# Performance work log

Measured on AMD Instinct MI355X. Metric: run time of the kernel, lower is better.

## Reference

```python
import jax, jax.numpy as jnp
import numpy as np

KH = KW = 3
STRIDE = 1
ITERATIONS = 2
EPS = 1e-7


def _squash(s):
    # squash along last axis (capsule dim)
    sn = jnp.sum(s * s, axis=-1, keepdims=True)
    return (sn / (1.0 + sn)) * s / jnp.sqrt(sn + EPS)


def setup_inputs() -> dict:
    key = jax.random.key(0)
    k1, k2 = jax.random.split(key)
    x = jax.random.normal(k1, (4, 14, 14, 32, 8), dtype=jnp.float32)
    # W: [1,1,1,filters_out, caps_per_patch=3*3*32, dims_out=16, dims_in=8], stddev=0.1 init
    W = 0.1 * jax.random.normal(k2, (1, 1, 1, 32, 288, 16, 8), dtype=jnp.float32)
    return {"x": x, "W": W}


def reference(x, W):
    B, H, Wd, Fin, Din = x.shape
    Ho = (H - KH) // STRIDE + 1
    Wo = (Wd - KW) // STRIDE + 1
    # Patch extraction, channel order (kh, kw, Fin) to match tf.image.extract_patches
    patches = jnp.stack(
        [x[:, i:i + Ho * STRIDE:STRIDE, j:j + Wo * STRIDE:STRIDE]
         for i in range(KH) for j in range(KW)],
        axis=3,
    )  # [B,Ho,Wo,KH*KW,Fin,Din]
    patches = patches.reshape(B, Ho, Wo, KH * KW * Fin, Din)  # [B,Ho,Wo,C,Di]

    Wm = W[0, 0, 0]  # [F, C, Do, Di]
    F, C, Do, _ = Wm.shape
    # predictions[b,h,w,f,c,o] = sum_i W[f,c,o,i] * patches[b,h,w,c,i]
    preds = jnp.einsum('fcoi,bhwci->bhwfco', Wm, patches)

    logits = jnp.zeros((B, Ho, Wo, F, C), dtype=preds.dtype)
    outputs = jnp.zeros((B, Ho, Wo, F, Do), dtype=preds.dtype)
    for _ in range(ITERATIONS):
        # agreement = predictions^T @ outputs over the dims_out axis
        agreement = jnp.einsum('bhwfco,bhwfo->bhwfc', preds, outputs)
        logits = logits + agreement
        # NOTE: original code softmaxes over axis=3 (the filters_out axis)
        cc = jax.nn.softmax(logits, axis=3)  # [B,Ho,Wo,F,C]
        centroids = jnp.sum(cc[..., None] * preds, axis=4)  # [B,Ho,Wo,F,Do]
        outputs = _squash(centroids)
    return outputs
```

## Files before the change

### kernel.cpp

```cpp
#include <hip/hip_runtime.h>

#define NB   4
#define H_IN 14
#define W_IN 14
#define FIN  32
#define DI   8
#define F    32
#define C    288
#define DO   16
#define HO   12
#define WO   12
#define NPOS (NB*HO*WO)
#define EPS  1e-7f

#define CH   16
#define CC   (C/CH)
#define GP   4
#define GRID (CH*(NPOS/GP))

#define XELE  (NB*H_IN*W_IN*FIN*DI)
#define W2H_BYTES  ((size_t)F*C*DO*DI*2)
#define XH_BYTES   ((size_t)XELE*2)
#define CENT_BYTES ((size_t)NPOS*F*DO*4)
#define PART_BYTES ((size_t)CH*CENT_BYTES)
#define OUT1_BYTES CENT_BYTES

#define WBLK ((F*C*DO)/256)
#define XBLK ((XELE/4 + 255)/256)

typedef _Float16 h2 __attribute__((ext_vector_type(2)));

__device__ __forceinline__ unsigned int pack2(float a, float b) {
    h2 v; v.x = (_Float16)a; v.y = (_Float16)b;
    return __builtin_bit_cast(unsigned int, v);
}

__device__ __forceinline__ float dot8h(const uint4 w, const uint4 v, float acc) {
#if __has_builtin(__builtin_amdgcn_fdot2)
    acc = __builtin_amdgcn_fdot2(__builtin_bit_cast(h2, w.x), __builtin_bit_cast(h2, v.x), acc, false);
    acc = __builtin_amdgcn_fdot2(__builtin_bit_cast(h2, w.y), __builtin_bit_cast(h2, v.y), acc, false);
    acc = __builtin_amdgcn_fdot2(__builtin_bit_cast(h2, w.z), __builtin_bit_cast(h2, v.z), acc, false);
    acc = __builtin_amdgcn_fdot2(__builtin_bit_cast(h2, w.w), __builtin_bit_cast(h2, v.w), acc, false);
#else
    const h2 w0 = __builtin_bit_cast(h2, w.x), v0 = __builtin_bit_cast(h2, v.x);
    const h2 w1 = __builtin_bit_cast(h2, w.y), v1 = __builtin_bit_cast(h2, v.y);
    const h2 w2 = __builtin_bit_cast(h2, w.z), v2 = __builtin_bit_cast(h2, v.z);
    const h2 w3 = __builtin_bit_cast(h2, w.w), v3 = __builtin_bit_cast(h2, v.w);
    acc += (float)w0.x*(float)v0.x + (float)w0.y*(float)v0.y
         + (float)w1.x*(float)v1.x + (float)w1.y*(float)v1.y
         + (float)w2.x*(float)v2.x + (float)w2.y*(float)v2.y
         + (float)w3.x*(float)v3.x + (float)w3.y*(float)v3.y;
#endif
    return acc;
}

__device__ __forceinline__ int xbase_of(int pos) {
    const int b = pos/(HO*WO), rem = pos%(HO*WO), ho = rem/WO, wo = rem%WO;
    return ((b*H_IN + ho)*W_IN + wo)*FIN*DI;
}

__device__ __forceinline__ int coff_of(int c) {
    const int slab = c >> 5, fin = c & 31;
    const int kh = slab/3, kw = slab%3;
    return (kh*W_IN + kw)*FIN*DI + fin*DI;
}

__global__ __launch_bounds__(256) void kernConv(const float* __restrict__ Wt,
                                                unsigned short* __restrict__ W2h,
                                                const float* __restrict__ x,
                                                unsigned short* __restrict__ xh) {
    const int b = blockIdx.x;
    if (b < WBLK) {
        const int idx = b*256 + threadIdx.x;
        const int f = idx & 31, o = (idx >> 5) & 15, c = idx >> 9;
        const float* src = Wt + ((size_t)(f*C + c)*DO + o)*DI;
        const float4 a = *(const float4*)src;
        const float4 bb = *(const float4*)(src + 4);
        uint4 r;
        r.x = pack2(a.x, a.y);  r.y = pack2(a.z, a.w);
        r.z = pack2(bb.x, bb.y); r.w = pack2(bb.z, bb.w);
        ((uint4*)W2h)[idx] = r;
    } else {
        const int i = (b - WBLK)*256 + threadIdx.x;
        if (i < XELE/4) {
            const float4 v = ((const float4*)x)[i];
            uint2 o;
            o.x = pack2(v.x, v.y); o.y = pack2(v.z, v.w);
            ((uint2*)xh)[i] = o;
        }
    }
}

__global__ __launch_bounds__(256, 8) void kern1n(const unsigned short* __restrict__ xh,
                                                 const unsigned short* __restrict__ W2h,
                                                 float* __restrict__ part1)
{
    const int tid = threadIdx.x;
    const int f  = tid & 31;
    const int og = tid >> 5;
    const int o0 = 2*og, o1 = o0 + 1;
    const int ch = blockIdx.x & (CH-1);
    const int pg = blockIdx.x >> 4;

    int xoff[GP];
    #pragma unroll
    for (int p = 0; p < GP; ++p) xoff[p] = xbase_of(pg*GP + p);

    const uint4* W2h4 = (const uint4*)W2h;
    const int c0 = ch*CC;

    float acc0[GP], acc1[GP];
    #pragma unroll
    for (int p = 0; p < GP; ++p) { acc0[p] = 0.f; acc1[p] = 0.f; }

    #pragma unroll 1
    for (int cl = 0; cl < CC; ++cl) {
        const int c = c0 + cl;
        const int coff = coff_of(c);
        const uint4 w0 = W2h4[(size_t)(c*DO + o0)*F + f];
        const uint4 w1 = W2h4[(size_t)(c*DO + o1)*F + f];
        #pragma unroll
        for (int p = 0; p < GP; ++p) {
            const uint4 xv = *(const uint4*)(xh + xoff[p] + coff);
            acc0[p] = dot8h(w0, xv, acc0[p]);
            acc1[p] = dot8h(w1, xv, acc1[p]);
        }
    }
    #pragma unroll
    for (int p = 0; p < GP; ++p) {
        const size_t base = ((size_t)(ch*NPOS + pg*GP + p))*DO;
        part1[(base + o0)*F + f] = acc0[p];
        part1[(base + o1)*F + f] = acc1[p];
    }
}

__global__ __launch_bounds__(512) void kernO(const float* __restrict__ part1,
                                             float* __restrict__ out1)
{
    __shared__ float red[512];
    const int pos = blockIdx.x, tid = threadIdx.x;
    const int f = tid & 31, o = tid >> 5;

    float s = 0.f;
    #pragma unroll
    for (int k = 0; k < CH; ++k)
        s += part1[(size_t)(k*NPOS + pos)*512 + tid];
    s *= (1.f/32.f);

    red[tid] = s*s;
    __syncthreads();
    if (tid < 256) red[tid] += red[tid + 256];
    __syncthreads();
    if (tid < 128) red[tid] += red[tid + 128];
    __syncthreads();
    if (tid < 64)  red[tid] += red[tid + 64];
    __syncthreads();
    if (tid < 32) {
        const float sn = red[tid] + red[tid + 32];
        red[tid] = (sn/(1.f + sn)) * rsqrtf(sn + EPS);
    }
    __syncthreads();
    out1[(size_t)pos*512 + f*DO + o] = s * red[f];
}

__global__ __launch_bounds__(256, 8) void kern2n(const unsigned short* __restrict__ xh,
                                                 const unsigned short* __restrict__ W2h,
                                                 const float* __restrict__ out1,
                                                 float* __restrict__ part2)
{
    __shared__ float red[2][4][GP][32];
    __shared__ float ccs[2][GP][32];

    const int tid = threadIdx.x;
    const int f  = tid & 31;
    const int og = tid >> 5;
    const int o0 = 2*og, o1 = o0 + 1;
    const int wv = tid >> 6;
    const int half = (tid >> 5) & 1;
    const int ch = blockIdx.x & (CH-1);
    const int pg = blockIdx.x >> 4;

    int xoff[GP];
    #pragma unroll
    for (int p = 0; p < GP; ++p) xoff[p] = xbase_of(pg*GP + p);

    float u0[GP], u1[GP];
    #pragma unroll
    for (int p = 0; p < GP; ++p) {
        const float* up = out1 + (size_t)(pg*GP + p)*512 + f*DO;
        u0[p] = up[o0];
        u1[p] = up[o1];
    }

    const uint4* W2h4 = (const uint4*)W2h;
    const int c0 = ch*CC;

    float acc0[GP], acc1[GP];
    #pragma unroll
    for (int p = 0; p < GP; ++p) { acc0[p] = 0.f; acc1[p] = 0.f; }

    #pragma unroll 1
    for (int cl = 0; cl < CC; ++cl) {
        const int c = c0 + cl;
        const int buf = cl & 1;
        const int coff = coff_of(c);
        const uint4 w0 = W2h4[(size_t)(c*DO + o0)*F + f];
        const uint4 w1 = W2h4[(size_t)(c*DO + o1)*F + f];

        float pred0[GP], pred1[GP];
        #pragma unroll
        for (int p = 0; p < GP; ++p) {
            const uint4 xv = *(const uint4*)(xh + xoff[p] + coff);
            pred0[p] = dot8h(w0, xv, 0.f);
            pred1[p] = dot8h(w1, xv, 0.f);
        }

        #pragma unroll
        for (int p = 0; p < GP; ++p) {
            float ap = pred0[p]*u0[p] + pred1[p]*u1[p];
            ap += __shfl_xor(ap, 32);
            if (half == 0) red[buf][wv][p][f] = ap;
        }
        __syncthreads();

        {
            const int p2 = tid >> 5, f2 = tid & 31;
            if (p2 < GP) {
                const float agr = red[buf][0][p2][f2] + red[buf][1][p2][f2]
                                + red[buf][2][p2][f2] + red[buf][3][p2][f2];
                float m = agr;
                m = fmaxf(m, __shfl_xor(m, 1));
                m = fmaxf(m, __shfl_xor(m, 2));
                m = fmaxf(m, __shfl_xor(m, 4));
                m = fmaxf(m, __shfl_xor(m, 8));
                m = fmaxf(m, __shfl_xor(m, 16));
                const float e = __expf(agr - m);
                float s = e;
                s += __shfl_xor(s, 1);
                s += __shfl_xor(s, 2);
                s += __shfl_xor(s, 4);
                s += __shfl_xor(s, 8);
                s += __shfl_xor(s, 16);
                ccs[buf][p2][f2] = e / s;
            }
        }
        __syncthreads();

        #pragma unroll
        for (int p = 0; p < GP; ++p) {
            const float cv = ccs[buf][p][f];
            acc0[p] += cv*pred0[p];
            acc1[p] += cv*pred1[p];
        }
    }

    #pragma unroll
    for (int p = 0; p < GP; ++p) {
        const size_t base = ((size_t)(ch*NPOS + pg*GP + p))*DO;
        part2[(base + o0)*F + f] = acc0[p];
        part2[(base + o1)*F + f] = acc1[p];
    }
}

__global__ __launch_bounds__(256) void kern3(const float* __restrict__ part2,
                                             float* __restrict__ out)
{
    const int tid = threadIdx.x;
    const int f = tid & 31, p = tid >> 5;
    const int pos = blockIdx.x*8 + p;

    float cent[DO];
    #pragma unroll
    for (int o = 0; o < DO; ++o) cent[o] = 0.f;
    #pragma unroll 1
    for (int k = 0; k < CH; ++k) {
        const float* s = part2 + (size_t)(k*NPOS + pos)*512 + f;
        #pragma unroll
        for (int o = 0; o < DO; ++o) cent[o] += s[o*F];
    }
    float sn = 0.f;
    #pragma unroll
    for (int o = 0; o < DO; ++o) sn += cent[o]*cent[o];
    const float sc = (sn/(1.f + sn)) * rsqrtf(sn + EPS);
    float* dst = out + ((size_t)pos*F + f)*DO;
    #pragma unroll
    for (int o = 0; o < DO; ++o) dst[o] = cent[o]*sc;
}

__device__ __forceinline__ float dot8(const float4* __restrict__ w,
                                      const float4 p0, const float4 p1) {
    float4 a = w[0], b = w[1];
    return a.x*p0.x + a.y*p0.y + a.z*p0.z + a.w*p0.w
         + b.x*p1.x + b.y*p1.y + b.z*p1.z + b.w*p1.w;
}

__global__ __launch_bounds__(256) void capsule_kernel_f32(
    const float* __restrict__ x, const float* __restrict__ Wt,
    float* __restrict__ out)
{
    __shared__ float patch[C*DI];
    __shared__ float cent[F*DO];
    __shared__ float out1[F*DO];
    __shared__ float agr[F*C];
    __shared__ float scale_s[F];

    const int tid = threadIdx.x;
    const int pos = blockIdx.x;
    const int b   = pos / (HO*WO);
    const int rem = pos % (HO*WO);
    const int ho  = rem / WO;
    const int wo  = rem % WO;

    #pragma unroll
    for (int slab = 0; slab < 9; ++slab) {
        const int kh = slab / 3, kw = slab % 3;
        const float* src = x + (((b*H_IN + ho + kh)*W_IN + (wo + kw))*FIN)*DI;
        patch[slab*256 + tid] = src[tid];
    }
    __syncthreads();

    const float4* pv = (const float4*)patch;

    {
        const int fo0 = tid, fo1 = tid + 256;
        const int f0 = fo0 >> 4, o0 = fo0 & 15;
        const int f1 = fo1 >> 4, o1 = fo1 & 15;
        float acc0 = 0.f, acc1 = 0.f;
        for (int c = 0; c < C; ++c) {
            const float4 p0 = pv[c*2], p1 = pv[c*2+1];
            acc0 += dot8((const float4*)(Wt + ((f0*C + c)*DO + o0)*DI), p0, p1);
            acc1 += dot8((const float4*)(Wt + ((f1*C + c)*DO + o1)*DI), p0, p1);
        }
        cent[fo0] = acc0 * (1.f/32.f);
        cent[fo1] = acc1 * (1.f/32.f);
    }
    __syncthreads();

    if (tid < F) {
        float sn = 0.f;
        #pragma unroll
        for (int o = 0; o < DO; ++o) { float v = cent[tid*DO + o]; sn += v*v; }
        const float sc = (sn/(1.f + sn)) * rsqrtf(sn + EPS);
        #pragma unroll
        for (int o = 0; o < DO; ++o) out1[tid*DO + o] = cent[tid*DO + o] * sc;
    }
    __syncthreads();

    #pragma unroll 1
    for (int r = 0; r < (F*C)/256; ++r) {
        const int pp = tid + 256*r;
        const int f = pp / C, c = pp % C;
        const float4* wrow = (const float4*)(Wt + (f*C + c)*DO*DI);
        const float4 p0 = pv[c*2], p1 = pv[c*2+1];
        float a = 0.f;
        #pragma unroll
        for (int o = 0; o < DO; ++o) a += dot8(wrow + o*2, p0, p1) * out1[f*DO + o];
        agr[pp] = a;
    }
    __syncthreads();

    for (int c = tid; c < C; c += 256) {
        float m = -1e30f;
        #pragma unroll
        for (int f = 0; f < F; ++f) m = fmaxf(m, agr[f*C + c]);
        float s = 0.f;
        #pragma unroll
        for (int f = 0; f < F; ++f) {
            const float e = __expf(agr[f*C + c] - m);
            agr[f*C + c] = e; s += e;
        }
        const float inv = 1.f / s;
        #pragma unroll
        for (int f = 0; f < F; ++f) agr[f*C + c] *= inv;
    }
    __syncthreads();

    {
        const int fo0 = tid, fo1 = tid + 256;
        const int f0 = fo0 >> 4, o0 = fo0 & 15;
        const int f1 = fo1 >> 4, o1 = fo1 & 15;
        float acc0 = 0.f, acc1 = 0.f;
        for (int c = 0; c < C; ++c) {
            const float4 p0 = pv[c*2], p1 = pv[c*2+1];
            acc0 += agr[f0*C + c] * dot8((const float4*)(Wt + ((f0*C + c)*DO + o0)*DI), p0, p1);
            acc1 += agr[f1*C + c] * dot8((const float4*)(Wt + ((f1*C + c)*DO + o1)*DI), p0, p1);
        }
        cent[fo0] = acc0;
        cent[fo1] = acc1;
    }
    __syncthreads();

    if (tid < F) {
        float sn = 0.f;
        #pragma unroll
        for (int o = 0; o < DO; ++o) { float v = cent[tid*DO + o]; sn += v*v; }
        scale_s[tid] = (sn/(1.f + sn)) * rsqrtf(sn + EPS);
    }
    __syncthreads();

    out[pos*(F*DO) + tid]       = cent[tid]       * scale_s[tid >> 4];
    out[pos*(F*DO) + tid + 256] = cent[tid + 256] * scale_s[(tid >> 4) + 16];
}

extern "C" void kernel_launch(void* const* d_in, const int* in_sizes, int n_in,
                              void* d_out, int out_size, void* d_ws, size_t ws_size,
                              hipStream_t stream) {
    const float* x  = (const float*)d_in[0];
    const float* Wt = (const float*)d_in[1];
    float* out = (float*)d_out;

    if (ws_size >= W2H_BYTES + XH_BYTES + PART_BYTES + OUT1_BYTES) {
        unsigned short* W2h = (unsigned short*)d_ws;
        unsigned short* xh  = (unsigned short*)((char*)d_ws + W2H_BYTES);
        float* part = (float*)((char*)d_ws + W2H_BYTES + XH_BYTES);
        float* out1 = (float*)((char*)d_ws + W2H_BYTES + XH_BYTES + PART_BYTES);
        kernConv<<<WBLK + XBLK, 256, 0, stream>>>(Wt, W2h, x, xh);
        kern1n<<<GRID, 256, 0, stream>>>(xh, W2h, part);
        kernO<<<NPOS, 512, 0, stream>>>(part, out1);
        kern2n<<<GRID, 256, 0, stream>>>(xh, W2h, out1, part);
        kern3<<<NPOS/8, 256, 0, stream>>>(part, out);
    } else {
        capsule_kernel_f32<<<NPOS, 256, 0, stream>>>(x, Wt, out);
    }
}
```

Baseline: 144.9 us.

## Compute first routing iteration with MFMA over pre-extracted fp16 patches

Replaces the first-iteration dot-product kernel and its separate reduce/squash kernel with one MFMA-based kernel. It computes the uniform-weight centroid as a GEMM over all 288×8 inputs per filter and fuses the squash in-register. The conversion kernel now also writes a plain fp16 copy of W and a materialized fp16 patch matrix, and kern2n reads the patch matrix with linear offsets. GP doubles to 8, so the softmax stage uses all threads. The cost is a larger workspace and extra conversion traffic, and kern2n now carries more per-thread state.

```diff
diff --git a/kernel.cpp b/kernel.cpp
--- a/kernel.cpp
+++ b/kernel.cpp
@@ -15,20 +15,25 @@
 
 #define CH   16
 #define CC   (C/CH)
-#define GP   4
+#define GP   8
 #define GRID (CH*(NPOS/GP))
 
-#define XELE  (NB*H_IN*W_IN*FIN*DI)
+#define KTOT (C*DI)
+
 #define W2H_BYTES  ((size_t)F*C*DO*DI*2)
-#define XH_BYTES   ((size_t)XELE*2)
-#define CENT_BYTES ((size_t)NPOS*F*DO*4)
-#define PART_BYTES ((size_t)CH*CENT_BYTES)
-#define OUT1_BYTES CENT_BYTES
-
-#define WBLK ((F*C*DO)/256)
-#define XBLK ((XELE/4 + 255)/256)
+#define WH_BYTES   ((size_t)F*C*DO*DI*2)
+#define PH_BYTES   ((size_t)NPOS*KTOT*2)
+#define PART_BYTES ((size_t)CH*NPOS*F*DO*4)
+#define OUT1_BYTES ((size_t)NPOS*F*DO*4)
+
+#define CVT_W2H 576
+#define CVT_WH  576
+#define CVT_PH  648
+#define CVT_GRID (CVT_W2H + CVT_WH + CVT_PH)
 
 typedef _Float16 h2 __attribute__((ext_vector_type(2)));
+typedef _Float16 h8v __attribute__((ext_vector_type(8)));
+typedef float    f4v __attribute__((ext_vector_type(4)));
 
 __device__ __forceinline__ unsigned int pack2(float a, float b) {
     h2 v; v.x = (_Float16)a; v.y = (_Float16)b;
@@ -66,107 +71,85 @@
 }
 
 __global__ __launch_bounds__(256) void kernConv(const float* __restrict__ Wt,
+                                                const float* __restrict__ x,
                                                 unsigned short* __restrict__ W2h,
-                                                const float* __restrict__ x,
-                                                unsigned short* __restrict__ xh) {
+                                                unsigned short* __restrict__ Wh,
+                                                unsigned short* __restrict__ Ph) {
     const int b = blockIdx.x;
-    if (b < WBLK) {
+    if (b < CVT_W2H) {
         const int idx = b*256 + threadIdx.x;
         const int f = idx & 31, o = (idx >> 5) & 15, c = idx >> 9;
         const float* src = Wt + ((size_t)(f*C + c)*DO + o)*DI;
         const float4 a = *(const float4*)src;
         const float4 bb = *(const float4*)(src + 4);
         uint4 r;
-        r.x = pack2(a.x, a.y);  r.y = pack2(a.z, a.w);
+        r.x = pack2(a.x, a.y);   r.y = pack2(a.z, a.w);
         r.z = pack2(bb.x, bb.y); r.w = pack2(bb.z, bb.w);
         ((uint4*)W2h)[idx] = r;
+    } else if (b < CVT_W2H + CVT_WH) {
+        const int idx = (b - CVT_W2H)*256 + threadIdx.x;
+        const float* src = Wt + (size_t)idx*8;
+        const float4 a = *(const float4*)src;
+        const float4 bb = *(const float4*)(src + 4);
+        uint4 r;
+        r.x = pack2(a.x, a.y);   r.y = pack2(a.z, a.w);
+        r.z = pack2(bb.x, bb.y); r.w = pack2(bb.z, bb.w);
+        ((uint4*)Wh)[idx] = r;
     } else {
-        const int i = (b - WBLK)*256 + threadIdx.x;
-        if (i < XELE/4) {
-            const float4 v = ((const float4*)x)[i];
-            uint2 o;
-            o.x = pack2(v.x, v.y); o.y = pack2(v.z, v.w);
-            ((uint2*)xh)[i] = o;
-        }
-    }
-}
-
-__global__ __launch_bounds__(256, 8) void kern1n(const unsigned short* __restrict__ xh,
-                                                 const unsigned short* __restrict__ W2h,
-                                                 float* __restrict__ part1)
+        const int pc = (b - CVT_W2H - CVT_WH)*256 + threadIdx.x;
+        const int pos = pc / C, c = pc % C;
+        const float* src = x + xbase_of(pos) + coff_of(c);
+        const float4 a = *(const float4*)src;
+        const float4 bb = *(const float4*)(src + 4);
+        uint4 r;
+        r.x = pack2(a.x, a.y);   r.y = pack2(a.z, a.w);
+        r.z = pack2(bb.x, bb.y); r.w = pack2(bb.z, bb.w);
+        ((uint4*)Ph)[pc] = r;
+    }
+}
+
+__global__ __launch_bounds__(256) void kernM1(const unsigned short* __restrict__ Ph,
+                                              const unsigned short* __restrict__ Wh,
+                                              float* __restrict__ out1)
 {
-    const int tid = threadIdx.x;
-    const int f  = tid & 31;
-    const int og = tid >> 5;
-    const int o0 = 2*og, o1 = o0 + 1;
-    const int ch = blockIdx.x & (CH-1);
-    const int pg = blockIdx.x >> 4;
-
-    int xoff[GP];
-    #pragma unroll
-    for (int p = 0; p < GP; ++p) xoff[p] = xbase_of(pg*GP + p);
-
-    const uint4* W2h4 = (const uint4*)W2h;
-    const int c0 = ch*CC;
-
-    float acc0[GP], acc1[GP];
-    #pragma unroll
-    for (int p = 0; p < GP; ++p) { acc0[p] = 0.f; acc1[p] = 0.f; }
-
-    #pragma unroll 1
-    for (int cl = 0; cl < CC; ++cl) {
-        const int c = c0 + cl;
-        const int coff = coff_of(c);
-        const uint4 w0 = W2h4[(size_t)(c*DO + o0)*F + f];
-        const uint4 w1 = W2h4[(size_t)(c*DO + o1)*F + f];
-        #pragma unroll
-        for (int p = 0; p < GP; ++p) {
-            const uint4 xv = *(const uint4*)(xh + xoff[p] + coff);
-            acc0[p] = dot8h(w0, xv, acc0[p]);
-            acc1[p] = dot8h(w1, xv, acc1[p]);
-        }
-    }
-    #pragma unroll
-    for (int p = 0; p < GP; ++p) {
-        const size_t base = ((size_t)(ch*NPOS + pg*GP + p))*DO;
-        part1[(base + o0)*F + f] = acc0[p];
-        part1[(base + o1)*F + f] = acc1[p];
-    }
-}
-
-__global__ __launch_bounds__(512) void kernO(const float* __restrict__ part1,
-                                             float* __restrict__ out1)
-{
-    __shared__ float red[512];
-    const int pos = blockIdx.x, tid = threadIdx.x;
-    const int f = tid & 31, o = tid >> 5;
-
-    float s = 0.f;
-    #pragma unroll
-    for (int k = 0; k < CH; ++k)
-        s += part1[(size_t)(k*NPOS + pos)*512 + tid];
-    s *= (1.f/32.f);
-
-    red[tid] = s*s;
-    __syncthreads();
-    if (tid < 256) red[tid] += red[tid + 256];
-    __syncthreads();
-    if (tid < 128) red[tid] += red[tid + 128];
-    __syncthreads();
-    if (tid < 64)  red[tid] += red[tid + 64];
-    __syncthreads();
-    if (tid < 32) {
-        const float sn = red[tid] + red[tid + 32];
-        red[tid] = (sn/(1.f + sn)) * rsqrtf(sn + EPS);
-    }
-    __syncthreads();
-    out1[(size_t)pos*512 + f*DO + o] = s * red[f];
-}
-
-__global__ __launch_bounds__(256, 8) void kern2n(const unsigned short* __restrict__ xh,
-                                                 const unsigned short* __restrict__ W2h,
-                                                 const float* __restrict__ out1,
-                                                 float* __restrict__ part2)
+    const int lane = threadIdx.x & 63;
+    const int wv   = threadIdx.x >> 6;
+    const int f    = blockIdx.x & 31;
+    const int pt   = (blockIdx.x >> 5)*4 + wv;
+    const int pos0 = pt*16;
+    const int n    = lane & 15, q = lane >> 4;
+
+    const unsigned short* pa = Ph + (size_t)(pos0 + n)*KTOT + q*8;
+    const unsigned short* pb = Wh + ((size_t)(f*C + q)*DO + n)*DI;
+
+    f4v acc0 = {0.f,0.f,0.f,0.f}, acc1 = {0.f,0.f,0.f,0.f};
+    #pragma unroll 4
+    for (int s = 0; s < KTOT/32; s += 2) {
+        const h8v a0 = *(const h8v*)(pa + (size_t)s*32);
+        const h8v b0 = *(const h8v*)(pb + (size_t)s*4*DO*DI);
+        const h8v a1 = *(const h8v*)(pa + (size_t)(s+1)*32);
+        const h8v b1 = *(const h8v*)(pb + (size_t)(s+1)*4*DO*DI);
+        acc0 = __builtin_amdgcn_mfma_f32_16x16x32_f16(a0, b0, acc0, 0, 0, 0);
+        acc1 = __builtin_amdgcn_mfma_f32_16x16x32_f16(a1, b1, acc1, 0, 0, 0);
+    }
+
+    #pragma unroll
+    for (int r = 0; r < 4; ++r) {
+        const float v = (acc0[r] + acc1[r]) * (1.f/32.f);
+        float sq = v*v;
+        sq += __shfl_xor(sq, 1);
+        sq += __shfl_xor(sq, 2);
+        sq += __shfl_xor(sq, 4);
+        sq += __shfl_xor(sq, 8);
+        const float sc = (sq/(1.f + sq)) * rsqrtf(sq + EPS);
+        out1[(size_t)(pos0 + q*4 + r)*512 + f*DO + n] = v * sc;
+    }
+}
+
+__global__ __launch_bounds__(256) void kern2n(const unsigned short* __restrict__ Ph,
+                                              const unsigned short* __restrict__ W2h,
+                                              const float* __restrict__ out1,
+                                              float* __restrict__ part2)
 {
     __shared__ float red[2][4][GP][32];
     __shared__ float ccs[2][GP][32];
@@ -180,9 +163,9 @@
     const int ch = blockIdx.x & (CH-1);
     const int pg = blockIdx.x >> 4;
 
-    int xoff[GP];
-    #pragma unroll
-    for (int p = 0; p < GP; ++p) xoff[p] = xbase_of(pg*GP + p);
+    int poff[GP];
+    #pragma unroll
+    for (int p = 0; p < GP; ++p) poff[p] = (pg*GP + p)*KTOT;
 
     float u0[GP], u1[GP];
     #pragma unroll
@@ -203,14 +186,13 @@
     for (int cl = 0; cl < CC; ++cl) {
         const int c = c0 + cl;
         const int buf = cl & 1;
-        const int coff = coff_of(c);
         const uint4 w0 = W2h4[(size_t)(c*DO + o0)*F + f];
         const uint4 w1 = W2h4[(size_t)(c*DO + o1)*F + f];
 
         float pred0[GP], pred1[GP];
         #pragma unroll
         for (int p = 0; p < GP; ++p) {
-            const uint4 xv = *(const uint4*)(xh + xoff[p] + coff);
+            const uint4 xv = *(const uint4*)(Ph + poff[p] + c*DI);
             pred0[p] = dot8h(w0, xv, 0.f);
             pred1[p] = dot8h(w1, xv, 0.f);
         }
@@ -225,24 +207,22 @@
 
         {
             const int p2 = tid >> 5, f2 = tid & 31;
-            if (p2 < GP) {
-                const float agr = red[buf][0][p2][f2] + red[buf][1][p2][f2]
-                                + red[buf][2][p2][f2] + red[buf][3][p2][f2];
-                float m = agr;
-                m = fmaxf(m, __shfl_xor(m, 1));
-                m = fmaxf(m, __shfl_xor(m, 2));
-                m = fmaxf(m, __shfl_xor(m, 4));
-                m = fmaxf(m, __shfl_xor(m, 8));
-                m = fmaxf(m, __shfl_xor(m, 16));
-                const float e = __expf(agr - m);
-                float s = e;
-                s += __shfl_xor(s, 1);
-                s += __shfl_xor(s, 2);
-                s += __shfl_xor(s, 4);
-                s += __shfl_xor(s, 8);
-                s += __shfl_xor(s, 16);
-                ccs[buf][p2][f2] = e / s;
-            }
+            const float agr = red[buf][0][p2][f2] + red[buf][1][p2][f2]
+                            + red[buf][2][p2][f2] + red[buf][3][p2][f2];
+            float m = agr;
+            m = fmaxf(m, __shfl_xor(m, 1));
+            m = fmaxf(m, __shfl_xor(m, 2));
+            m = fmaxf(m, __shfl_xor(m, 4));
+            m = fmaxf(m, __shfl_xor(m, 8));
+            m = fmaxf(m, __shfl_xor(m, 16));
+            const float e = __expf(agr - m);
+            float s = e;
+            s += __shfl_xor(s, 1);
+            s += __shfl_xor(s, 2);
+            s += __shfl_xor(s, 4);
+            s += __shfl_xor(s, 8);
+            s += __shfl_xor(s, 16);
+            ccs[buf][p2][f2] = e / s;
         }
         __syncthreads();
 
@@ -409,15 +389,17 @@
     const float* Wt = (const float*)d_in[1];
     float* out = (float*)d_out;
 
-    if (ws_size >= W2H_BYTES + XH_BYTES + PART_BYTES + OUT1_BYTES) {
-        unsigned short* W2h = (unsigned short*)d_ws;
-        unsigned short* xh  = (unsigned short*)((char*)d_ws + W2H_BYTES);
-        float* part = (float*)((char*)d_ws + W2H_BYTES + XH_BYTES);
-        float* out1 = (float*)((char*)d_ws + W2H_BYTES + XH_BYTES + PART_BYTES);
-        kernConv<<<WBLK + XBLK, 256, 0, stream>>>(Wt, W2h, x, xh);
-        kern1n<<<GRID, 256, 0, stream>>>(xh, W2h, part);
-        kernO<<<NPOS, 512, 0, stream>>>(part, out1);
-        kern2n<<<GRID, 256, 0, stream>>>(xh, W2h, out1, part);
+    if (ws_size >= W2H_BYTES + WH_BYTES + PH_BYTES + PART_BYTES + OUT1_BYTES) {
+        char* p = (char*)d_ws;
+        unsigned short* W2h = (unsigned short*)p;            p += W2H_BYTES;
+        unsigned short* Wh  = (unsigned short*)p;            p += WH_BYTES;
+        unsigned short* Ph  = (unsigned short*)p;            p += PH_BYTES;
+        float* part = (float*)p;                             p += PART_BYTES;
+        float* out1 = (float*)p;
+
+        kernConv<<<CVT_GRID, 256, 0, stream>>>(Wt, x, W2h, Wh, Ph);
+        kernM1<<<(F/1)*9, 256, 0, stream>>>(Ph, Wh, out1);
+        kern2n<<<GRID, 256, 0, stream>>>(Ph, W2h, out1, part);
         kern3<<<NPOS/8, 256, 0, stream>>>(part, out);
     } else {
         capsule_kernel_f32<<<NPOS, 256, 0, stream>>>(x, Wt, out);
```

New measurement: 138.1 us. 1.05x faster.
